# Optimization experiments

Hardware: AMD Instinct MI355X
Metric: run time of the kernel (lower is better)

Reference implementation:

```python
import jax, jax.numpy as jnp
import numpy as np

N_NODES = 100000
N_EDGES = 1250000
IN_CH = 64
OUT_CH = 64


def setup_inputs() -> dict:
    key = jax.random.key(0)
    k1, k2, k3 = jax.random.split(key, 3)
    x = jax.random.normal(k1, (N_NODES, IN_CH), dtype=jnp.float32)
    edge_index = jax.random.randint(k2, (2, N_EDGES), 0, N_NODES, dtype=jnp.int64)
    # torch.nn.Linear(3*IN_CH, OUT_CH): W [out, in], b [out]
    scale = 1.0 / np.sqrt(3 * IN_CH)
    W = jax.random.uniform(k3, (OUT_CH, 3 * IN_CH), dtype=jnp.float32,
                           minval=-scale, maxval=scale)
    b = jnp.zeros((OUT_CH,), dtype=jnp.float32)
    return {"x": x, "edge_index": edge_index, "W": W, "b": b}


def reference(x, edge_index, W, b):
    src, dst = edge_index[0], edge_index[1]
    msgs = x[src]  # [E, D] gather of source node features

    agg_sum = jax.ops.segment_sum(msgs, dst, num_segments=N_NODES)  # [N, D]
    count = jax.ops.segment_sum(jnp.ones((msgs.shape[0],), dtype=x.dtype),
                                dst, num_segments=N_NODES)  # [N]
    agg_mean = agg_sum / jnp.maximum(count, 1.0)[:, None]

    agg_max = jax.ops.segment_max(msgs, dst, num_segments=N_NODES)  # [N, D]
    has_edge = (count > 0)[:, None]
    agg_max = jnp.where(has_edge, agg_max, 0.0)  # empty segments -> 0 (PyG default)

    feats = jnp.concatenate([agg_sum, agg_mean, agg_max], axis=-1)  # [N, 3D]
    return jnp.einsum('nf,of->no', feats, W) + b
```

## Files before the change

### kernel.cpp

```cpp
#include <hip/hip_runtime.h>
#include <hip/hip_bf16.h>
#include <math.h>

#define D    64
#define F3   192
#define FS   128
#define NPB  256
#define LBITS 8
#define SBITS 17
#define NBLK 256
#define SCAN_CHUNK 2048
#define BUCKET_PAD 1800
#define SSRC_CAP   2000000

using bf16x8 = __attribute__((ext_vector_type(8))) short;
using f32x4  = __attribute__((ext_vector_type(4))) float;

__device__ __forceinline__ ushort f2bf(float f) {
    __hip_bfloat16 h = __float2bfloat16(f);
    return *reinterpret_cast<ushort*>(&h);
}
__device__ __forceinline__ float bf2f(ushort u) {
    unsigned v = ((unsigned)u) << 16;
    return __uint_as_float(v);
}

__global__ __launch_bounds__(256) void k_cast_hist(
    const float* __restrict__ x, ushort* __restrict__ xb, int n4,
    const float* __restrict__ W, ushort* __restrict__ Wb, int nW,
    const int* __restrict__ dstv, unsigned* __restrict__ bcntT,
    int E, int EPB, int NB, int castBlocks)
{
    int bid = blockIdx.x;
    if (bid < NBLK) {
        __shared__ unsigned h[512];
        for (int i = threadIdx.x; i < NB; i += 256) h[i] = 0;
        __syncthreads();
        int lo = bid * EPB, hi = min(E, lo + EPB);
        for (int e = lo + threadIdx.x; e < hi; e += 256)
            atomicAdd(&h[((unsigned)dstv[e]) >> LBITS], 1u);
        __syncthreads();
        for (int i = threadIdx.x; i < NB; i += 256)
            bcntT[(size_t)i * NBLK + bid] = h[i];
    } else if (bid < NBLK + castBlocks) {
        int i = (bid - NBLK) * 256 + threadIdx.x;
        if (i < n4) {
            float4 v = *reinterpret_cast<const float4*>(x + (size_t)i * 4);
            ushort4 u = { f2bf(v.x), f2bf(v.y), f2bf(v.z), f2bf(v.w) };
            *reinterpret_cast<ushort4*>(xb + (size_t)i * 4) = u;
        }
    } else {
        for (int i = threadIdx.x; i < nW; i += 256) Wb[i] = f2bf(W[i]);
    }
}

__global__ __launch_bounds__(256) void k_chunk_scan(
    const unsigned* __restrict__ cnt, unsigned* __restrict__ offs,
    unsigned* __restrict__ partials, int N)
{
    __shared__ unsigned ts[256];
    int t = threadIdx.x;
    int ebase = blockIdx.x * SCAN_CHUNK + t * 8;
    unsigned v[8];
    unsigned s = 0;
    #pragma unroll
    for (int j = 0; j < 8; ++j) {
        unsigned c = (ebase + j < N) ? cnt[ebase + j] : 0u;
        v[j] = s; s += c;
    }
    ts[t] = s;
    __syncthreads();
    #pragma unroll
    for (int off = 1; off < 256; off <<= 1) {
        unsigned add = (t >= off) ? ts[t - off] : 0u;
        __syncthreads();
        ts[t] += add;
        __syncthreads();
    }
    unsigned tb = (t > 0) ? ts[t - 1] : 0u;
    #pragma unroll
    for (int j = 0; j < 8; ++j)
        if (ebase + j < N) offs[ebase + j] = tb + v[j];
    if (t == 255) partials[blockIdx.x] = ts[255];
}

__device__ __forceinline__ void scan_partials_lds(
    const unsigned* __restrict__ partials, unsigned* psc, int n, int t)
{
    __shared__ unsigned raw[64];
    if (t < n) raw[t] = partials[t];
    __syncthreads();
    if (t == 0) {
        unsigned s = 0;
        for (int i = 0; i < n; ++i) { unsigned c = raw[i]; psc[i] = s; s += c; }
    }
    __syncthreads();
}

__global__ __launch_bounds__(256) void k_bin_scatter(
    const int* __restrict__ srcv, const int* __restrict__ dstv,
    const unsigned* __restrict__ bbaseT, const unsigned* __restrict__ partials,
    int nChunks, unsigned* __restrict__ binned, int E, int EPB, int NB)
{
    __shared__ unsigned cur[512];
    __shared__ unsigned psc[64];
    int t = threadIdx.x;
    scan_partials_lds(partials, psc, nChunks, t);
    for (int i = t; i < NB; i += 256) {
        unsigned idx = (unsigned)i * NBLK + blockIdx.x;
        cur[i] = bbaseT[idx] + psc[idx >> 11];
    }
    __syncthreads();
    int lo = blockIdx.x * EPB, hi = min(E, lo + EPB);
    for (int e = lo + t; e < hi; e += 256) {
        unsigned d = (unsigned)dstv[e];
        unsigned s = (unsigned)srcv[e];
        unsigned p = atomicAdd(&cur[d >> LBITS], 1u);
        binned[p] = ((d & (NPB - 1u)) << SBITS) | s;
    }
}

__global__ __launch_bounds__(256) void k_bucket_csr(
    const unsigned* __restrict__ binned, const unsigned* __restrict__ bbaseT,
    const unsigned* __restrict__ partials, int nChunks,
    unsigned* __restrict__ offs, unsigned* __restrict__ cnt,
    unsigned* __restrict__ ssrc, int E, int NB, int N)
{
    __shared__ unsigned c[256];
    __shared__ unsigned ts[256];
    __shared__ unsigned psc[64];
    int k = blockIdx.x;
    int t = threadIdx.x;
    scan_partials_lds(partials, psc, nChunks, t);

    unsigned i0 = (unsigned)k * NBLK;
    unsigned bstart = bbaseT[i0] + psc[i0 >> 11];
    unsigned bend;
    if (k + 1 < NB) {
        unsigned i1 = (unsigned)(k + 1) * NBLK;
        bend = bbaseT[i1] + psc[i1 >> 11];
    } else bend = (unsigned)E;
    unsigned bstartPad = ((bstart + 7u) & ~7u) + (unsigned)BUCKET_PAD * k;

    c[t] = 0;
    __syncthreads();
    for (unsigned e = bstart + t; e < bend; e += 256)
        atomicAdd(&c[binned[e] >> SBITS], 1u);
    __syncthreads();

    unsigned myc  = c[t];
    unsigned mycp = (myc + 7u) & ~7u;
    ts[t] = mycp;
    __syncthreads();
    #pragma unroll
    for (int off = 1; off < 256; off <<= 1) {
        unsigned add = (t >= off) ? ts[t - off] : 0u;
        __syncthreads();
        ts[t] += add;
        __syncthreads();
    }
    unsigned exclp = t ? ts[t - 1] : 0u;
    unsigned stPad = bstartPad + exclp;

    int gn = k * NPB + t;
    if (gn < N) { offs[gn] = stPad; cnt[gn] = myc; }

    c[t] = exclp;
    __syncthreads();
    for (unsigned e = bstart + t; e < bend; e += 256) {
        unsigned u  = binned[e];
        unsigned ld = u >> SBITS;
        unsigned r  = atomicAdd(&c[ld], 1u);
        ssrc[bstartPad + r] = u & ((1u << SBITS) - 1u);
    }
    __syncthreads();
    if (myc && mycp > myc) {
        unsigned lastId = ssrc[stPad + myc - 1];
        for (unsigned j = myc; j < mycp; ++j) ssrc[stPad + j] = lastId;
    }
}

__global__ __launch_bounds__(256) void k_gather4(
    const ushort*   __restrict__ xb,
    const unsigned* __restrict__ ssrc,
    const unsigned* __restrict__ offs,
    const unsigned* __restrict__ cnt,
    ushort*         __restrict__ feats,
    int N)
{
    int tid  = threadIdx.x;
    unsigned lane = tid & 63;
    int wv   = tid >> 6;

    int n = blockIdx.x * 4 + wv;
    if (n >= N) return;

    unsigned st  = offs[n];
    unsigned dg  = cnt[n];
    unsigned dgp = (dg + 7u) & ~7u;

    float s = 0.0f, m = -INFINITY;
    for (unsigned i = 0; i < dgp; i += 8) {
        uint4 ia = *reinterpret_cast<const uint4*>(ssrc + st + i);
        uint4 ib = *reinterpret_cast<const uint4*>(ssrc + st + i + 4);
        float a0 = bf2f(xb[(ia.x << 6) | lane]);
        float a1 = bf2f(xb[(ia.y << 6) | lane]);
        float a2 = bf2f(xb[(ia.z << 6) | lane]);
        float a3 = bf2f(xb[(ia.w << 6) | lane]);
        float a4 = bf2f(xb[(ib.x << 6) | lane]);
        float a5 = bf2f(xb[(ib.y << 6) | lane]);
        float a6 = bf2f(xb[(ib.z << 6) | lane]);
        float a7 = bf2f(xb[(ib.w << 6) | lane]);
        s += ((a0 + a1) + (a2 + a3)) + ((a4 + a5) + (a6 + a7));
        m = fmaxf(m, fmaxf(fmaxf(fmaxf(a0, a1), fmaxf(a2, a3)),
                           fmaxf(fmaxf(a4, a5), fmaxf(a6, a7))));
    }
    unsigned p = dgp - dg;
    if (p && dg) {
        unsigned lastId = ssrc[st + dg - 1];
        float last = bf2f(xb[(lastId << 6) | lane]);
        s -= (float)p * last;
    }

    size_t fb = (size_t)n * FS;
    feats[fb + lane]      = f2bf(s);
    feats[fb + 64 + lane] = dg ? f2bf(m) : (ushort)0;
}

__global__ __launch_bounds__(256) void k_mlp2(
    const ushort*   __restrict__ feats,
    const unsigned* __restrict__ cnt,
    const ushort*   __restrict__ Wb,
    const float*    __restrict__ bias,
    float*          __restrict__ out,
    int N)
{
    int tid  = threadIdx.x;
    int lane = tid & 63;
    int wv   = tid >> 6;
    int l16  = lane & 15;
    int kb   = (lane >> 4) << 3;

    int col = (wv << 4) + l16;
    const ushort* wp = Wb + (size_t)col * F3 + kb;
    bf16x8 bS0 = *reinterpret_cast<const bf16x8*>(wp);
    bf16x8 bS1 = *reinterpret_cast<const bf16x8*>(wp + 32);
    bf16x8 bM0 = *reinterpret_cast<const bf16x8*>(wp + 64);
    bf16x8 bM1 = *reinterpret_cast<const bf16x8*>(wp + 96);
    bf16x8 bX0 = *reinterpret_cast<const bf16x8*>(wp + 128);
    bf16x8 bX1 = *reinterpret_cast<const bf16x8*>(wp + 160);
    float bo = bias[col];

    int n0 = blockIdx.x << 4;

    unsigned dgr = cnt[n0 + l16];
    float inv = dgr ? 1.0f / (float)dgr : 0.0f;

    const ushort* arow = feats + (size_t)(n0 + l16) * FS + kb;
    bf16x8 aS0 = *reinterpret_cast<const bf16x8*>(arow);
    bf16x8 aS1 = *reinterpret_cast<const bf16x8*>(arow + 32);
    bf16x8 aX0 = *reinterpret_cast<const bf16x8*>(arow + 64);
    bf16x8 aX1 = *reinterpret_cast<const bf16x8*>(arow + 96);

    bf16x8 aM0, aM1;
    #pragma unroll
    for (int j = 0; j < 8; ++j) {
        aM0[j] = (short)f2bf(bf2f((ushort)aS0[j]) * inv);
        aM1[j] = (short)f2bf(bf2f((ushort)aS1[j]) * inv);
    }

    f32x4 acc = { bo, bo, bo, bo };
    acc = __builtin_amdgcn_mfma_f32_16x16x32_bf16(aS0, bS0, acc, 0, 0, 0);
    acc = __builtin_amdgcn_mfma_f32_16x16x32_bf16(aS1, bS1, acc, 0, 0, 0);
    acc = __builtin_amdgcn_mfma_f32_16x16x32_bf16(aM0, bM0, acc, 0, 0, 0);
    acc = __builtin_amdgcn_mfma_f32_16x16x32_bf16(aM1, bM1, acc, 0, 0, 0);
    acc = __builtin_amdgcn_mfma_f32_16x16x32_bf16(aX0, bX0, acc, 0, 0, 0);
    acc = __builtin_amdgcn_mfma_f32_16x16x32_bf16(aX1, bX1, acc, 0, 0, 0);

    int rbase = n0 + ((lane >> 4) << 2);
    #pragma unroll
    for (int r = 0; r < 4; ++r)
        out[(size_t)(rbase + r) * D + col] = acc[r];
}

extern "C" void kernel_launch(void* const* d_in, const int* in_sizes, int n_in,
                              void* d_out, int out_size, void* d_ws, size_t ws_size,
                              hipStream_t stream)
{
    const float* x  = (const float*)d_in[0];
    const int*   ei = (const int*)d_in[1];
    const float* W  = (const float*)d_in[2];
    const float* b  = (const float*)d_in[3];
    float* out = (float*)d_out;

    int N = in_sizes[0] / D;
    int E = in_sizes[1] / 2;
    const int* srcv = ei;
    const int* dstv = ei + E;

    int NB  = (N + NPB - 1) / NPB;
    int EPB = (E + NBLK - 1) / NBLK;
    int M   = NB * NBLK;

    unsigned* bcntT    = (unsigned*)d_ws;
    unsigned* bbaseT   = bcntT + M;
    unsigned* partials = bbaseT + M;
    unsigned* offs     = partials + 64;
    unsigned* cnt      = offs + N;
    unsigned* ssrc     = cnt + N;
    ushort*   xb       = (ushort*)(ssrc + SSRC_CAP);
    ushort*   Wb       = xb + (size_t)N * D;
    ushort*   feats    = Wb + (size_t)D * F3;
    unsigned* binned   = (unsigned*)feats;

    int nChunksM  = (M + SCAN_CHUNK - 1) / SCAN_CHUNK;
    int n4        = N * D / 4;
    int castBlocks = (n4 + 255) / 256;

    k_cast_hist<<<NBLK + castBlocks + 1, 256, 0, stream>>>(
        x, xb, n4, W, Wb, D * F3, dstv, bcntT, E, EPB, NB, castBlocks);
    k_chunk_scan<<<nChunksM, 256, 0, stream>>>(bcntT, bbaseT, partials, M);
    k_bin_scatter<<<NBLK, 256, 0, stream>>>(srcv, dstv, bbaseT, partials,
                                            nChunksM, binned, E, EPB, NB);
    k_bucket_csr<<<NB, 256, 0, stream>>>(binned, bbaseT, partials, nChunksM,
                                         offs, cnt, ssrc, E, NB, N);
    k_gather4<<<(N + 3) / 4, 256, 0, stream>>>(xb, ssrc, offs, cnt, feats, N);
    k_mlp2<<<N / 16, 256, 0, stream>>>(feats, cnt, Wb, b, out, N);
}
```

Before: 123.5 us.

## Gather two edges per wave with 32-bit loads and a persistent grid

Rewrites the gather-aggregate kernel so each half-wave reads a different source row, using 32-bit loads that cover two bf16 channels. The two halves are combined with a cross-lane shuffle, and the output is written as packed 32-bit words. The kernel now runs as a grid-stride loop over 2048 blocks and unrolls by 16 edges with split accumulators. The aim is to cut load instruction count and per-node launch overhead, at the cost of extra shuffle and select work.

```diff
diff --git a/kernel.cpp b/kernel.cpp
--- a/kernel.cpp
+++ b/kernel.cpp
@@ -180,7 +180,7 @@
     }
 }
 
-__global__ __launch_bounds__(256) void k_gather4(
+__global__ __launch_bounds__(256) void k_gather5(
     const ushort*   __restrict__ xb,
     const unsigned* __restrict__ ssrc,
     const unsigned* __restrict__ offs,
@@ -188,43 +188,111 @@
     ushort*         __restrict__ feats,
     int N)
 {
+    const unsigned* xw = reinterpret_cast<const unsigned*>(xb);
+    unsigned* fw = reinterpret_cast<unsigned*>(feats);
+
     int tid  = threadIdx.x;
     unsigned lane = tid & 63;
+    unsigned l31  = lane & 31;
+    bool     hi   = lane >= 32;
     int wv   = tid >> 6;
 
-    int n = blockIdx.x * 4 + wv;
-    if (n >= N) return;
-
-    unsigned st  = offs[n];
-    unsigned dg  = cnt[n];
-    unsigned dgp = (dg + 7u) & ~7u;
-
-    float s = 0.0f, m = -INFINITY;
-    for (unsigned i = 0; i < dgp; i += 8) {
-        uint4 ia = *reinterpret_cast<const uint4*>(ssrc + st + i);
-        uint4 ib = *reinterpret_cast<const uint4*>(ssrc + st + i + 4);
-        float a0 = bf2f(xb[(ia.x << 6) | lane]);
-        float a1 = bf2f(xb[(ia.y << 6) | lane]);
-        float a2 = bf2f(xb[(ia.z << 6) | lane]);
-        float a3 = bf2f(xb[(ia.w << 6) | lane]);
-        float a4 = bf2f(xb[(ib.x << 6) | lane]);
-        float a5 = bf2f(xb[(ib.y << 6) | lane]);
-        float a6 = bf2f(xb[(ib.z << 6) | lane]);
-        float a7 = bf2f(xb[(ib.w << 6) | lane]);
-        s += ((a0 + a1) + (a2 + a3)) + ((a4 + a5) + (a6 + a7));
-        m = fmaxf(m, fmaxf(fmaxf(fmaxf(a0, a1), fmaxf(a2, a3)),
-                           fmaxf(fmaxf(a4, a5), fmaxf(a6, a7))));
-    }
-    unsigned p = dgp - dg;
-    if (p && dg) {
-        unsigned lastId = ssrc[st + dg - 1];
-        float last = bf2f(xb[(lastId << 6) | lane]);
-        s -= (float)p * last;
-    }
-
-    size_t fb = (size_t)n * FS;
-    feats[fb + lane]      = f2bf(s);
-    feats[fb + 64 + lane] = dg ? f2bf(m) : (ushort)0;
+    int nq = (N + 3) >> 2;
+    for (int q = blockIdx.x; q < nq; q += gridDim.x) {
+        int n = q * 4 + wv;
+        if (n >= N) continue;
+
+        unsigned st  = offs[n];
+        unsigned dg  = cnt[n];
+        unsigned dgp = (dg + 7u) & ~7u;
+
+        float se0 = 0.f, so0 = 0.f, se1 = 0.f, so1 = 0.f;
+        float me0 = -INFINITY, mo0 = -INFINITY, me1 = -INFINITY, mo1 = -INFINITY;
+
+        unsigned i = 0;
+        for (; i + 16 <= dgp; i += 16) {
+            uint4 ia = *reinterpret_cast<const uint4*>(ssrc + st + i);
+            uint4 ib = *reinterpret_cast<const uint4*>(ssrc + st + i + 4);
+            uint4 ic = *reinterpret_cast<const uint4*>(ssrc + st + i + 8);
+            uint4 id = *reinterpret_cast<const uint4*>(ssrc + st + i + 12);
+            unsigned p0 = hi ? ia.y : ia.x;
+            unsigned p1 = hi ? ia.w : ia.z;
+            unsigned p2 = hi ? ib.y : ib.x;
+            unsigned p3 = hi ? ib.w : ib.z;
+            unsigned p4 = hi ? ic.y : ic.x;
+            unsigned p5 = hi ? ic.w : ic.z;
+            unsigned p6 = hi ? id.y : id.x;
+            unsigned p7 = hi ? id.w : id.z;
+            unsigned w0 = xw[(p0 << 5) | l31];
+            unsigned w1 = xw[(p1 << 5) | l31];
+            unsigned w2 = xw[(p2 << 5) | l31];
+            unsigned w3 = xw[(p3 << 5) | l31];
+            unsigned w4 = xw[(p4 << 5) | l31];
+            unsigned w5 = xw[(p5 << 5) | l31];
+            unsigned w6 = xw[(p6 << 5) | l31];
+            unsigned w7 = xw[(p7 << 5) | l31];
+            #pragma unroll
+            for (int j = 0; j < 8; ++j) {
+                unsigned w = (j==0)?w0:(j==1)?w1:(j==2)?w2:(j==3)?w3:
+                             (j==4)?w4:(j==5)?w5:(j==6)?w6:w7;
+                float fe = __uint_as_float(w << 16);
+                float fo = __uint_as_float(w & 0xFFFF0000u);
+                if (j & 1) {
+                    se1 += fe; so1 += fo;
+                    me1 = fmaxf(me1, fe); mo1 = fmaxf(mo1, fo);
+                } else {
+                    se0 += fe; so0 += fo;
+                    me0 = fmaxf(me0, fe); mo0 = fmaxf(mo0, fo);
+                }
+            }
+        }
+        if (i < dgp) {
+            uint4 ia = *reinterpret_cast<const uint4*>(ssrc + st + i);
+            uint4 ib = *reinterpret_cast<const uint4*>(ssrc + st + i + 4);
+            unsigned p0 = hi ? ia.y : ia.x;
+            unsigned p1 = hi ? ia.w : ia.z;
+            unsigned p2 = hi ? ib.y : ib.x;
+            unsigned p3 = hi ? ib.w : ib.z;
+            unsigned w0 = xw[(p0 << 5) | l31];
+            unsigned w1 = xw[(p1 << 5) | l31];
+            unsigned w2 = xw[(p2 << 5) | l31];
+            unsigned w3 = xw[(p3 << 5) | l31];
+            #pragma unroll
+            for (int j = 0; j < 4; ++j) {
+                unsigned w = (j==0)?w0:(j==1)?w1:(j==2)?w2:w3;
+                float fe = __uint_as_float(w << 16);
+                float fo = __uint_as_float(w & 0xFFFF0000u);
+                if (j & 1) {
+                    se1 += fe; so1 += fo;
+                    me1 = fmaxf(me1, fe); mo1 = fmaxf(mo1, fo);
+                } else {
+                    se0 += fe; so0 += fo;
+                    me0 = fmaxf(me0, fe); mo0 = fmaxf(mo0, fo);
+                }
+            }
+        }
+
+        float se = se0 + se1, so = so0 + so1;
+        float me = fmaxf(me0, me1), mo = fmaxf(mo0, mo1);
+        se += __shfl_xor(se, 32);
+        so += __shfl_xor(so, 32);
+        me = fmaxf(me, __shfl_xor(me, 32));
+        mo = fmaxf(mo, __shfl_xor(mo, 32));
+
+        unsigned p = dgp - dg;
+        if (p && dg) {
+            unsigned lastId = ssrc[st + dg - 1];
+            unsigned w = xw[(lastId << 5) | l31];
+            se -= (float)p * __uint_as_float(w << 16);
+            so -= (float)p * __uint_as_float(w & 0xFFFF0000u);
+        }
+        if (!dg) { me = 0.0f; mo = 0.0f; }
+
+        float v0 = hi ? me : se;
+        float v1 = hi ? mo : so;
+        unsigned outw = ((unsigned)f2bf(v0)) | (((unsigned)f2bf(v1)) << 16);
+        fw[((size_t)n << 6) | lane] = outw;
+    }
 }
 
 __global__ __launch_bounds__(256) void k_mlp2(
@@ -324,6 +392,6 @@
                                             nChunksM, binned, E, EPB, NB);
     k_bucket_csr<<<NB, 256, 0, stream>>>(binned, bbaseT, partials, nChunksM,
                                          offs, cnt, ssrc, E, NB, N);
-    k_gather4<<<(N + 3) / 4, 256, 0, stream>>>(xb, ssrc, offs, cnt, feats, N);
+    k_gather5<<<2048, 256, 0, stream>>>(xb, ssrc, offs, cnt, feats, N);
     k_mlp2<<<N / 16, 256, 0, stream>>>(feats, cnt, Wb, b, out, N);
 }
```

Result: faster. 114.4 us (median of 3 runs) (-7.3%).
